# Kernel tuning notes

Hardware: AMD Instinct MI355X
Metric: run time of the kernel (lower is better)

Reference implementation:

```python
import jax, jax.numpy as jnp
import numpy as np

N, EM, EW, L, S = 20000, 100000, 25000, 128, 6


def _mlp(x, W1, b1, W2, b2, g, beta):
    # Linear -> ReLU -> Linear -> LayerNorm
    h = jax.nn.relu(x @ W1 + b1) @ W2 + b2
    mu = jnp.mean(h, axis=-1, keepdims=True)
    var = jnp.mean((h - mu) ** 2, axis=-1, keepdims=True)
    return g * (h - mu) * jax.lax.rsqrt(var + 1e-5) + beta


def _scatter_mean(attr, recv, n):
    s = jax.ops.segment_sum(attr, recv, num_segments=n)
    c = jax.ops.segment_sum(jnp.ones((attr.shape[0], 1), attr.dtype), recv, num_segments=n)
    return s / jnp.maximum(c, 1.0)


def setup_inputs() -> dict:
    key = jax.random.key(0)
    ks = jax.random.split(key, 16)

    def w(k, shape, fan_in):
        return (jax.random.normal(k, shape, jnp.float32) / np.sqrt(fan_in).astype(np.float32))

    inp = {
        'x': jax.random.normal(ks[0], (N, L), jnp.float32),
        'mesh_edge_attr': jax.random.normal(ks[1], (EM, L), jnp.float32),
        'world_edge_attr': jax.random.normal(ks[2], (EW, L), jnp.float32),
        'mesh_edge_index': jax.random.randint(ks[3], (2, EM), 0, N),
        'world_edge_index': jax.random.randint(ks[4], (2, EW), 0, N),
    }
    i = 5
    for pre in ('me', 'we', 'nd'):
        inp[pre + '_W1'] = w(ks[i], (S, 3 * L, L), 3 * L); i += 1
        inp[pre + '_b1'] = jnp.zeros((S, L), jnp.float32)
        inp[pre + '_W2'] = w(ks[i], (S, L, L), L); i += 1
        inp[pre + '_b2'] = jnp.zeros((S, L), jnp.float32)
        inp[pre + '_g'] = jnp.ones((S, L), jnp.float32)
        inp[pre + '_beta'] = jnp.zeros((S, L), jnp.float32)
    return inp


def reference(x, mesh_edge_attr, world_edge_attr, mesh_edge_index, world_edge_index,
              me_W1, me_b1, me_W2, me_b2, me_g, me_beta,
              we_W1, we_b1, we_W2, we_b2, we_g, we_beta,
              nd_W1, nd_b1, nd_W2, nd_b2, nd_g, nd_beta):
    ms, mr = mesh_edge_index[0], mesh_edge_index[1]
    ws, wr = world_edge_index[0], world_edge_index[1]
    n = x.shape[0]

    def step(carry, p):
        x, mea, wea = carry
        (mW1, mb1, mW2, mb2, mg, mbe,
         wW1, wb1, wW2, wb2, wg, wbe,
         nW1, nb1, nW2, nb2, ng, nbe) = p
        # EdgeModel: gather + concat + MLP, residual into edge attrs
        mea = mea + _mlp(jnp.concatenate([x[ms], x[mr], mea], axis=-1), mW1, mb1, mW2, mb2, mg, mbe)
        wea = wea + _mlp(jnp.concatenate([x[ws], x[wr], wea], axis=-1), wW1, wb1, wW2, wb2, wg, wbe)
        # NodeModel: scatter-mean over both edge sets + concat + MLP, residual
        agg = jnp.concatenate([x, _scatter_mean(mea, mr, n), _scatter_mean(wea, wr, n)], axis=-1)
        x = x + _mlp(agg, nW1, nb1, nW2, nb2, ng, nbe)
        return (x, mea, wea), None

    params = (me_W1, me_b1, me_W2, me_b2, me_g, me_beta,
              we_W1, we_b1, we_W2, we_b2, we_g, we_beta,
              nd_W1, nd_b1, nd_W2, nd_b2, nd_g, nd_beta)
    (x, mea, wea), _ = jax.lax.scan(step, (x, mesh_edge_attr, world_edge_attr), params)
    return x, mea, wea
```

## Files before the change

### kernel.cpp

```cpp
#include <hip/hip_runtime.h>

constexpr int LDIM  = 128;
constexpr int NNODE = 20000;
constexpr int EM_N  = 100000;
constexpr int EW_N  = 25000;
constexpr int NSTEP = 6;

typedef short bf16x8 __attribute__((ext_vector_type(8)));
typedef short bf16x4 __attribute__((ext_vector_type(4)));
typedef float f32x4  __attribute__((ext_vector_type(4)));

struct MlpParams {
  const short* xb;
  const float* attrIn;
  float*       attrOut;
  short*       xbOut;
  const int*   src;
  const int*   dst;
  const float* gsrc1;
  const float* gsrc2;
  const int*   off1;
  const int*   csr1;
  const int*   off2;
  const int*   csr2;
  const short* W1H;
  const short* W2H;
  const short* W2L;
  const float* b1;
  const float* b2;
  const float* gam;
  const float* bet;
  int nRows;
};

__device__ __forceinline__ short f2b(float f) {
  unsigned int u = __float_as_uint(f);
  u = (u + 0x7fffu + ((u >> 16) & 1u)) >> 16;
  return (short)u;
}
__device__ __forceinline__ float b2f(short s) {
  return __uint_as_float(((unsigned int)(unsigned short)s) << 16);
}
__device__ __forceinline__ bf16x4 cvt4(float4 a, float sc) {
  bf16x4 o;
  o[0] = f2b(a.x * sc); o[1] = f2b(a.y * sc);
  o[2] = f2b(a.z * sc); o[3] = f2b(a.w * sc);
  return o;
}
__device__ __forceinline__ bf16x4 cvt4v(f32x4 a, float sc) {
  bf16x4 o;
  o[0] = f2b(a[0] * sc); o[1] = f2b(a[1] * sc);
  o[2] = f2b(a[2] * sc); o[3] = f2b(a[3] * sc);
  return o;
}

__launch_bounds__(256, 2)
__global__ void edge_kernel(MlpParams pmA, MlpParams pmB, int blocksA) {
  const bool isA = (int)blockIdx.x < blocksA;
  const MlpParams P = isA ? pmA : pmB;
  const int bid  = isA ? (int)blockIdx.x : (int)blockIdx.x - blocksA;
  const int row0 = bid * 128;

  __shared__ __align__(16) short Abuf[128][40];
  __shared__ __align__(16) short Bhi[128][40];
  __shared__ __align__(16) short Blo[128][40];
  __shared__ __align__(16) short Hbuf[128][136];
  __shared__ float b1s[128], b2s[128], gs[128], bes[128];
  __shared__ int   idxa[128], idxb[128];
  __shared__ float sumL[2][128], sqL[2][128];
  __shared__ float muL[128], rsL[128];

  const int t = threadIdx.x;

  if (t < 128) {
    b1s[t] = P.b1[t];
    gs[t]  = P.gam[t];
    int r = row0 + t;
    idxa[t] = (r < P.nRows) ? P.src[r] : 0;
  } else {
    int t2 = t - 128;
    b2s[t2] = P.b2[t2];
    bes[t2] = P.bet[t2];
    int r = row0 + t2;
    idxb[t2] = (r < P.nRows) ? P.dst[r] : 0;
  }
  __syncthreads();

  const int l   = t & 63;
  const int wid = t >> 6;
  const int wr  = wid >> 1, wcc = wid & 1;
  const int lr  = l & 15,  lg  = l >> 4;

  const int  srow  = t >> 1, sh = t & 1;
  const int  sgRow = row0 + srow;
  const bool sval  = sgRow < P.nRows;
  const int  sgC   = sval ? sgRow : 0;
  const float vmask = sval ? 1.f : 0.f;

  const short* bx0   = P.xb + (size_t)idxa[srow] * LDIM + sh * 16;
  const short* bx1   = P.xb + (size_t)idxb[srow] * LDIM + sh * 16;
  const float* base2 = P.attrIn + (size_t)sgC * LDIM + sh * 16;

  const int wrow = t >> 1, wsh = t & 1;
  const short* w1base = P.W1H + (size_t)wrow * 384 + wsh * 16;

  f32x4 acc[4][4];
#pragma unroll
  for (int i = 0; i < 4; ++i)
#pragma unroll
    for (int j = 0; j < 4; ++j) acc[i][j] = f32x4{0.f, 0.f, 0.f, 0.f};

  const bf16x8 z8 = {0, 0, 0, 0, 0, 0, 0, 0};
  bf16x8 pB0, pB1;
  float4 pA0, pA1, pA2, pA3;
  bf16x8 pW0, pW1;
  {
    pB0 = *(const bf16x8*)bx0;
    pB1 = *(const bf16x8*)(bx0 + 8);
    pW0 = *(const bf16x8*)w1base;
    pW1 = *(const bf16x8*)(w1base + 8);
  }

#pragma unroll
  for (int kc = 0; kc < 12; ++kc) {
    const int seg = kc >> 2;
    if (kc > 0) __syncthreads();
    {
      if (seg < 2) {
        *(bf16x8*)&Abuf[srow][sh * 16]     = sval ? pB0 : z8;
        *(bf16x8*)&Abuf[srow][sh * 16 + 8] = sval ? pB1 : z8;
      } else {
        *(bf16x4*)&Abuf[srow][sh * 16 + 0]  = cvt4(pA0, vmask);
        *(bf16x4*)&Abuf[srow][sh * 16 + 4]  = cvt4(pA1, vmask);
        *(bf16x4*)&Abuf[srow][sh * 16 + 8]  = cvt4(pA2, vmask);
        *(bf16x4*)&Abuf[srow][sh * 16 + 12] = cvt4(pA3, vmask);
      }
      *(bf16x8*)&Bhi[wrow][wsh * 16]     = pW0;
      *(bf16x8*)&Bhi[wrow][wsh * 16 + 8] = pW1;
    }
    __syncthreads();
    if (kc < 11) {
      const int kn = kc + 1, segn = kn >> 2, partn = kn & 3;
      if (segn == 0) {
        pB0 = *(const bf16x8*)(bx0 + partn * 32);
        pB1 = *(const bf16x8*)(bx0 + partn * 32 + 8);
      } else if (segn == 1) {
        pB0 = *(const bf16x8*)(bx1 + partn * 32);
        pB1 = *(const bf16x8*)(bx1 + partn * 32 + 8);
      } else {
        const float4* bp = (const float4*)(base2 + partn * 32);
        pA0 = bp[0]; pA1 = bp[1]; pA2 = bp[2]; pA3 = bp[3];
      }
      pW0 = *(const bf16x8*)(w1base + kn * 32);
      pW1 = *(const bf16x8*)(w1base + kn * 32 + 8);
    }
    bf16x8 av[4], bh[4];
#pragma unroll
    for (int mi = 0; mi < 4; ++mi)
      av[mi] = *(const bf16x8*)&Abuf[wr * 64 + mi * 16 + lr][lg * 8];
#pragma unroll
    for (int ni = 0; ni < 4; ++ni)
      bh[ni] = *(const bf16x8*)&Bhi[wcc * 64 + ni * 16 + lr][lg * 8];
#pragma unroll
    for (int mi = 0; mi < 4; ++mi)
#pragma unroll
      for (int ni = 0; ni < 4; ++ni)
        acc[mi][ni] = __builtin_amdgcn_mfma_f32_16x16x32_bf16(av[mi], bh[ni], acc[mi][ni], 0, 0, 0);
  }

#pragma unroll
  for (int rt = 0; rt < 4; ++rt)
#pragma unroll
    for (int ct = 0; ct < 4; ++ct) {
      const int cc = wcc * 64 + ct * 16 + lr;
      const float bb = b1s[cc];
#pragma unroll
      for (int q = 0; q < 4; ++q) {
        const int rr = wr * 64 + rt * 16 + lg * 4 + q;
        Hbuf[rr][cc] = f2b(fmaxf(acc[rt][ct][q] + bb, 0.f));
      }
    }

  f32x4 acc2[4][4];
#pragma unroll
  for (int i = 0; i < 4; ++i)
#pragma unroll
    for (int j = 0; j < 4; ++j) acc2[i][j] = f32x4{0.f, 0.f, 0.f, 0.f};

  const short* w2hbase = P.W2H + (size_t)wrow * 128 + wsh * 16;
  const short* w2lbase = P.W2L + (size_t)wrow * 128 + wsh * 16;

  bf16x8 qh0 = *(const bf16x8*)w2hbase;
  bf16x8 qh1 = *(const bf16x8*)(w2hbase + 8);
  bf16x8 ql0 = *(const bf16x8*)w2lbase;
  bf16x8 ql1 = *(const bf16x8*)(w2lbase + 8);

#pragma unroll
  for (int kc = 0; kc < 4; ++kc) {
    __syncthreads();
    {
      *(bf16x8*)&Bhi[wrow][wsh * 16]     = qh0;
      *(bf16x8*)&Bhi[wrow][wsh * 16 + 8] = qh1;
      *(bf16x8*)&Blo[wrow][wsh * 16]     = ql0;
      *(bf16x8*)&Blo[wrow][wsh * 16 + 8] = ql1;
    }
    __syncthreads();
    if (kc < 3) {
      qh0 = *(const bf16x8*)(w2hbase + (kc + 1) * 32);
      qh1 = *(const bf16x8*)(w2hbase + (kc + 1) * 32 + 8);
      ql0 = *(const bf16x8*)(w2lbase + (kc + 1) * 32);
      ql1 = *(const bf16x8*)(w2lbase + (kc + 1) * 32 + 8);
    }
    bf16x8 av2[4], bh2[4], bl2[4];
#pragma unroll
    for (int rt = 0; rt < 4; ++rt)
      av2[rt] = *(const bf16x8*)&Hbuf[wr * 64 + rt * 16 + lr][kc * 32 + lg * 8];
#pragma unroll
    for (int ct = 0; ct < 4; ++ct) {
      bh2[ct] = *(const bf16x8*)&Bhi[wcc * 64 + ct * 16 + lr][lg * 8];
      bl2[ct] = *(const bf16x8*)&Blo[wcc * 64 + ct * 16 + lr][lg * 8];
    }
#pragma unroll
    for (int rt = 0; rt < 4; ++rt)
#pragma unroll
      for (int ct = 0; ct < 4; ++ct) {
        acc2[rt][ct] = __builtin_amdgcn_mfma_f32_16x16x32_bf16(av2[rt], bl2[ct], acc2[rt][ct], 0, 0, 0);
        acc2[rt][ct] = __builtin_amdgcn_mfma_f32_16x16x32_bf16(av2[rt], bh2[ct], acc2[rt][ct], 0, 0, 0);
      }
  }

  float s1[4][4], s2[4][4];
#pragma unroll
  for (int rt = 0; rt < 4; ++rt)
#pragma unroll
    for (int q = 0; q < 4; ++q) { s1[rt][q] = 0.f; s2[rt][q] = 0.f; }
#pragma unroll
  for (int rt = 0; rt < 4; ++rt)
#pragma unroll
    for (int ct = 0; ct < 4; ++ct) {
      const float bb = b2s[wcc * 64 + ct * 16 + lr];
#pragma unroll
      for (int q = 0; q < 4; ++q) {
        float v = acc2[rt][ct][q] + bb;
        acc2[rt][ct][q] = v;
        s1[rt][q] += v;
        s2[rt][q] += v * v;
      }
    }
#pragma unroll
  for (int m = 1; m < 16; m <<= 1) {
#pragma unroll
    for (int rt = 0; rt < 4; ++rt)
#pragma unroll
      for (int q = 0; q < 4; ++q) {
        s1[rt][q] += __shfl_xor(s1[rt][q], m);
        s2[rt][q] += __shfl_xor(s2[rt][q], m);
      }
  }
  __syncthreads();
  {
    const int rt = lr >> 2, q = lr & 3;
    const int rr = wr * 64 + rt * 16 + lg * 4 + q;
    sumL[wcc][rr] = s1[rt][q];
    sqL[wcc][rr]  = s2[rt][q];
  }
  __syncthreads();
  if (t < 128) {
    const float tot = sumL[0][t] + sumL[1][t];
    const float tsq = sqL[0][t] + sqL[1][t];
    const float mu  = tot * (1.0f / 128.0f);
    const float var = tsq * (1.0f / 128.0f) - mu * mu;
    muL[t] = mu;
    rsL[t] = rsqrtf(var + 1e-5f);
  }
  __syncthreads();

#pragma unroll
  for (int rt = 0; rt < 4; ++rt) {
#pragma unroll
    for (int q = 0; q < 4; ++q) {
      const int rr = wr * 64 + rt * 16 + lg * 4 + q;
      const int grow = row0 + rr;
      if (grow < P.nRows) {
        const float mu = muL[rr], rs = rsL[rr];
        const float* rin = P.attrIn + (size_t)grow * LDIM;
        float* rout = P.attrOut + (size_t)grow * LDIM;
#pragma unroll
        for (int ct = 0; ct < 4; ++ct) {
          const int cc = wcc * 64 + ct * 16 + lr;
          rout[cc] = gs[cc] * (acc2[rt][ct][q] - mu) * rs + bes[cc] + rin[cc];
        }
      }
    }
  }
}

__launch_bounds__(256, 2)
__global__ void node_kernel(MlpParams P) {
  const int bid  = (int)blockIdx.x;
  const int row0 = bid * 128;

  __shared__ __align__(16) short Abuf[128][40];
  __shared__ __align__(16) short Bhi[128][40];
  __shared__ __align__(16) short Blo[128][40];
  __shared__ __align__(16) short Hbuf[128][136];
  __shared__ float b1s[128], b2s[128], gs[128], bes[128];
  __shared__ float sumL[2][128], sqL[2][128];
  __shared__ float muL[128], rsL[128];

  const int t = threadIdx.x;
  if (t < 128) { b1s[t] = P.b1[t]; gs[t] = P.gam[t]; }
  else         { b2s[t - 128] = P.b2[t - 128]; bes[t - 128] = P.bet[t - 128]; }

  const int l   = t & 63;
  const int wid = t >> 6;
  const int wr  = wid >> 1, wcc = wid & 1;
  const int lr  = l & 15,  lg  = l >> 4;

  const int  srow  = t >> 1, sh = t & 1;
  const int  sgRow = row0 + srow;
  const bool sval  = sgRow < P.nRows;
  const int  sgC   = sval ? sgRow : 0;

  const int wrow = t >> 1, wsh = t & 1;
  const short* w1base = P.W1H + (size_t)wrow * 384 + wsh * 16;
  const short* xrow   = P.xb + (size_t)sgC * LDIM + sh * 16;
  const bf16x8 z8 = {0, 0, 0, 0, 0, 0, 0, 0};

  f32x4 acc[4][4];
#pragma unroll
  for (int i = 0; i < 4; ++i)
#pragma unroll
    for (int j = 0; j < 4; ++j) acc[i][j] = f32x4{0.f, 0.f, 0.f, 0.f};

  f32x4 g[16];
#pragma unroll
  for (int j = 0; j < 16; ++j) g[j] = f32x4{0.f, 0.f, 0.f, 0.f};
  float scm = 1.f;
  {
    int beg = 0, end = 0;
    if (sval) { beg = P.off1[sgRow]; end = P.off1[sgRow + 1]; }
    for (int i = beg; i < end; ++i) {
      const float* er = P.gsrc1 + (size_t)P.csr1[i] * LDIM + sh * 16;
#pragma unroll
      for (int part = 0; part < 4; ++part) {
        const f32x4* p = (const f32x4*)(er + part * 32);
#pragma unroll
        for (int j = 0; j < 4; ++j) g[part * 4 + j] += p[j];
      }
    }
    scm = 1.0f / (float)max(end - beg, 1);
  }

  __syncthreads();

  float scw = 1.f;
#pragma unroll
  for (int kc = 0; kc < 12; ++kc) {
    const int seg = kc >> 2, part = kc & 3;
    if (kc > 0) __syncthreads();
    {
      if (seg == 0) {
        const bf16x8* xp = (const bf16x8*)(xrow + part * 32);
        *(bf16x8*)&Abuf[srow][sh * 16]     = sval ? xp[0] : z8;
        *(bf16x8*)&Abuf[srow][sh * 16 + 8] = sval ? xp[1] : z8;
      } else {
        const float sc = (seg == 1) ? scm : scw;
        *(bf16x4*)&Abuf[srow][sh * 16 + 0]  = cvt4v(g[part * 4 + 0], sc);
        *(bf16x4*)&Abuf[srow][sh * 16 + 4]  = cvt4v(g[part * 4 + 1], sc);
        *(bf16x4*)&Abuf[srow][sh * 16 + 8]  = cvt4v(g[part * 4 + 2], sc);
        *(bf16x4*)&Abuf[srow][sh * 16 + 12] = cvt4v(g[part * 4 + 3], sc);
      }
      const short* wsrc = w1base + kc * 32;
      *(bf16x8*)&Bhi[wrow][wsh * 16]     = *(const bf16x8*)wsrc;
      *(bf16x8*)&Bhi[wrow][wsh * 16 + 8] = *(const bf16x8*)(wsrc + 8);
      if (kc == 7) {
#pragma unroll
        for (int j = 0; j < 16; ++j) g[j] = f32x4{0.f, 0.f, 0.f, 0.f};
        int beg = 0, end = 0;
        if (sval) { beg = P.off2[sgRow]; end = P.off2[sgRow + 1]; }
        for (int i = beg; i < end; ++i) {
          const float* er = P.gsrc2 + (size_t)P.csr2[i] * LDIM + sh * 16;
#pragma unroll
          for (int pp = 0; pp < 4; ++pp) {
            const f32x4* p = (const f32x4*)(er + pp * 32);
#pragma unroll
            for (int j = 0; j < 4; ++j) g[pp * 4 + j] += p[j];
          }
        }
        scw = 1.0f / (float)max(end - beg, 1);
      }
    }
    __syncthreads();
    bf16x8 av[4], bh[4];
#pragma unroll
    for (int mi = 0; mi < 4; ++mi)
      av[mi] = *(const bf16x8*)&Abuf[wr * 64 + mi * 16 + lr][lg * 8];
#pragma unroll
    for (int ni = 0; ni < 4; ++ni)
      bh[ni] = *(const bf16x8*)&Bhi[wcc * 64 + ni * 16 + lr][lg * 8];
#pragma unroll
    for (int mi = 0; mi < 4; ++mi)
#pragma unroll
      for (int ni = 0; ni < 4; ++ni)
        acc[mi][ni] = __builtin_amdgcn_mfma_f32_16x16x32_bf16(av[mi], bh[ni], acc[mi][ni], 0, 0, 0);
  }

#pragma unroll
  for (int rt = 0; rt < 4; ++rt)
#pragma unroll
    for (int ct = 0; ct < 4; ++ct) {
      const int cc = wcc * 64 + ct * 16 + lr;
      const float bb = b1s[cc];
#pragma unroll
      for (int q = 0; q < 4; ++q) {
        const int rr = wr * 64 + rt * 16 + lg * 4 + q;
        Hbuf[rr][cc] = f2b(fmaxf(acc[rt][ct][q] + bb, 0.f));
      }
    }

  f32x4 acc2[4][4];
#pragma unroll
  for (int i = 0; i < 4; ++i)
#pragma unroll
    for (int j = 0; j < 4; ++j) acc2[i][j] = f32x4{0.f, 0.f, 0.f, 0.f};

  const short* w2hbase = P.W2H + (size_t)wrow * 128 + wsh * 16;
  const short* w2lbase = P.W2L + (size_t)wrow * 128 + wsh * 16;
  bf16x8 qh0 = *(const bf16x8*)w2hbase;
  bf16x8 qh1 = *(const bf16x8*)(w2hbase + 8);
  bf16x8 ql0 = *(const bf16x8*)w2lbase;
  bf16x8 ql1 = *(const bf16x8*)(w2lbase + 8);

#pragma unroll
  for (int kc = 0; kc < 4; ++kc) {
    __syncthreads();
    {
      *(bf16x8*)&Bhi[wrow][wsh * 16]     = qh0;
      *(bf16x8*)&Bhi[wrow][wsh * 16 + 8] = qh1;
      *(bf16x8*)&Blo[wrow][wsh * 16]     = ql0;
      *(bf16x8*)&Blo[wrow][wsh * 16 + 8] = ql1;
    }
    __syncthreads();
    if (kc < 3) {
      qh0 = *(const bf16x8*)(w2hbase + (kc + 1) * 32);
      qh1 = *(const bf16x8*)(w2hbase + (kc + 1) * 32 + 8);
      ql0 = *(const bf16x8*)(w2lbase + (kc + 1) * 32);
      ql1 = *(const bf16x8*)(w2lbase + (kc + 1) * 32 + 8);
    }
    bf16x8 av2[4], bh2[4], bl2[4];
#pragma unroll
    for (int rt = 0; rt < 4; ++rt)
      av2[rt] = *(const bf16x8*)&Hbuf[wr * 64 + rt * 16 + lr][kc * 32 + lg * 8];
#pragma unroll
    for (int ct = 0; ct < 4; ++ct) {
      bh2[ct] = *(const bf16x8*)&Bhi[wcc * 64 + ct * 16 + lr][lg * 8];
      bl2[ct] = *(const bf16x8*)&Blo[wcc * 64 + ct * 16 + lr][lg * 8];
    }
#pragma unroll
    for (int rt = 0; rt < 4; ++rt)
#pragma unroll
      for (int ct = 0; ct < 4; ++ct) {
        acc2[rt][ct] = __builtin_amdgcn_mfma_f32_16x16x32_bf16(av2[rt], bl2[ct], acc2[rt][ct], 0, 0, 0);
        acc2[rt][ct] = __builtin_amdgcn_mfma_f32_16x16x32_bf16(av2[rt], bh2[ct], acc2[rt][ct], 0, 0, 0);
      }
  }

  float s1[4][4], s2[4][4];
#pragma unroll
  for (int rt = 0; rt < 4; ++rt)
#pragma unroll
    for (int q = 0; q < 4; ++q) { s1[rt][q] = 0.f; s2[rt][q] = 0.f; }
#pragma unroll
  for (int rt = 0; rt < 4; ++rt)
#pragma unroll
    for (int ct = 0; ct < 4; ++ct) {
      const float bb = b2s[wcc * 64 + ct * 16 + lr];
#pragma unroll
      for (int q = 0; q < 4; ++q) {
        float v = acc2[rt][ct][q] + bb;
        acc2[rt][ct][q] = v;
        s1[rt][q] += v;
        s2[rt][q] += v * v;
      }
    }
#pragma unroll
  for (int m = 1; m < 16; m <<= 1) {
#pragma unroll
    for (int rt = 0; rt < 4; ++rt)
#pragma unroll
      for (int q = 0; q < 4; ++q) {
        s1[rt][q] += __shfl_xor(s1[rt][q], m);
        s2[rt][q] += __shfl_xor(s2[rt][q], m);
      }
  }
  __syncthreads();
  {
    const int rt = lr >> 2, q = lr & 3;
    const int rr = wr * 64 + rt * 16 + lg * 4 + q;
    sumL[wcc][rr] = s1[rt][q];
    sqL[wcc][rr]  = s2[rt][q];
  }
  __syncthreads();
  if (t < 128) {
    const float tot = sumL[0][t] + sumL[1][t];
    const float tsq = sqL[0][t] + sqL[1][t];
    const float mu  = tot * (1.0f / 128.0f);
    const float var = tsq * (1.0f / 128.0f) - mu * mu;
    muL[t] = mu;
    rsL[t] = rsqrtf(var + 1e-5f);
  }
  __syncthreads();

#pragma unroll
  for (int rt = 0; rt < 4; ++rt) {
#pragma unroll
    for (int q = 0; q < 4; ++q) {
      const int rr = wr * 64 + rt * 16 + lg * 4 + q;
      const int grow = row0 + rr;
      if (grow < P.nRows) {
        const float mu = muL[rr], rs = rsL[rr];
        const float* rin = P.attrIn + (size_t)grow * LDIM;
        float* rout = P.attrOut + (size_t)grow * LDIM;
        short* xbo  = P.xbOut + (size_t)grow * LDIM;
#pragma unroll
        for (int ct = 0; ct < 4; ++ct) {
          const int cc = wcc * 64 + ct * 16 + lr;
          const float o = gs[cc] * (acc2[rt][ct][q] - mu) * rs + bes[cc] + rin[cc];
          rout[cc] = o;
          xbo[cc] = f2b(o);
        }
      }
    }
  }
}

__global__ void prep_weights(const float* w1a, const float* w1b, const float* w1c,
                             const float* w2a, const float* w2b, const float* w2c,
                             short* w1h, short* w2h, short* w2l) {
  int i = blockIdx.x * 256 + threadIdx.x;
  constexpr int N1 = 18 * 128 * 384;
  constexpr int N2 = 18 * 128 * 128;
  if (i < N1) {
    int g = i / (128 * 384);
    int rem = i - g * (128 * 384);
    int n = rem / 384, k = rem - n * 384;
    int m = g / 6, s = g - m * 6;
    const float* src = (m == 0) ? w1a : (m == 1) ? w1b : w1c;
    w1h[i] = f2b(src[(size_t)s * (384 * 128) + (size_t)k * 128 + n]);
  } else if (i < N1 + N2) {
    int j = i - N1;
    int g = j / (128 * 128);
    int rem = j - g * (128 * 128);
    int n = rem / 128, k = rem - n * 128;
    int m = g / 6, s = g - m * 6;
    const float* src = (m == 0) ? w2a : (m == 1) ? w2b : w2c;
    float f = src[(size_t)s * (128 * 128) + (size_t)k * 128 + n];
    short hi = f2b(f);
    w2h[j] = hi;
    w2l[j] = f2b(f - b2f(hi));
  }
}

__global__ void prep_xb(const float* x, short* xb) {
  int i = blockIdx.x * 256 + threadIdx.x;
  if (i < NNODE * LDIM) xb[i] = f2b(x[i]);
}

__global__ void prep_deg(const int* mr, const int* wrcv, int* degm, int* degw) {
  int i = blockIdx.x * 256 + threadIdx.x;
  if (i < EM_N) atomicAdd(&degm[mr[i]], 1);
  else if (i < EM_N + EW_N) atomicAdd(&degw[wrcv[i - EM_N]], 1);
}

__global__ void prep_scan(const int* degm, const int* degw, int* moff, int* woff) {
  __shared__ int part[256];
  const int t = threadIdx.x;
  constexpr int NPT = (NNODE + 255) / 256;
#pragma unroll 1
  for (int pass = 0; pass < 2; ++pass) {
    const int* deg = pass == 0 ? degm : degw;
    int* off = pass == 0 ? moff : woff;
    int s = 0;
    for (int i = 0; i < NPT; ++i) {
      int n = t * NPT + i;
      if (n < NNODE) s += deg[n];
    }
    part[t] = s;
    __syncthreads();
    for (int d = 1; d < 256; d <<= 1) {
      int v = (t >= d) ? part[t - d] : 0;
      __syncthreads();
      part[t] += v;
      __syncthreads();
    }
    int base = (t == 0) ? 0 : part[t - 1];
    for (int i = 0; i < NPT; ++i) {
      int n = t * NPT + i;
      if (n < NNODE) { off[n] = base; base += deg[n]; }
    }
    if (t == 255) off[NNODE] = base;
    __syncthreads();
  }
}

__global__ void prep_fill(const int* mr, const int* wrcv,
                          const int* moff, const int* woff,
                          int* mcur, int* wcur, int* mcsr, int* wcsr) {
  int i = blockIdx.x * 256 + threadIdx.x;
  if (i < EM_N) {
    int d = mr[i];
    int pos = moff[d] + atomicAdd(&mcur[d], 1);
    mcsr[pos] = i;
  } else if (i < EM_N + EW_N) {
    int j = i - EM_N;
    int d = wrcv[j];
    int pos = woff[d] + atomicAdd(&wcur[d], 1);
    wcsr[pos] = j;
  }
}

extern "C" void kernel_launch(void* const* d_in, const int* in_sizes, int n_in,
                              void* d_out, int out_size, void* d_ws, size_t ws_size,
                              hipStream_t stream) {
  (void)in_sizes; (void)n_in; (void)out_size; (void)ws_size;
  const float* x_in   = (const float*)d_in[0];
  const float* mea_in = (const float*)d_in[1];
  const float* wea_in = (const float*)d_in[2];
  const int*   mei    = (const int*)d_in[3];
  const int*   wei    = (const int*)d_in[4];
  const float* W1s[3] = { (const float*)d_in[5],  (const float*)d_in[11], (const float*)d_in[17] };
  const float* B1s[3] = { (const float*)d_in[6],  (const float*)d_in[12], (const float*)d_in[18] };
  const float* W2s[3] = { (const float*)d_in[7],  (const float*)d_in[13], (const float*)d_in[19] };
  const float* B2s[3] = { (const float*)d_in[8],  (const float*)d_in[14], (const float*)d_in[20] };
  const float* Gs[3]  = { (const float*)d_in[9],  (const float*)d_in[15], (const float*)d_in[21] };
  const float* Be[3]  = { (const float*)d_in[10], (const float*)d_in[16], (const float*)d_in[22] };

  float* xo  = (float*)d_out;
  float* meo = xo  + (size_t)NNODE * LDIM;
  float* weo = meo + (size_t)EM_N * LDIM;

  int*   degm = (int*)d_ws;
  int*   degw = degm + NNODE;
  int*   mcur = degw + NNODE;
  int*   wcur = mcur + NNODE;
  int*   moff = wcur + NNODE;
  int*   woff = moff + (NNODE + 1);
  int*   mcsr = woff + (NNODE + 1);
  int*   wcsr = mcsr + EM_N;
  short* w1h  = (short*)(wcsr + EW_N);
  short* w2h  = w1h + (size_t)18 * 128 * 384;
  short* w2l  = w2h + (size_t)18 * 128 * 128;
  short* xb   = w2l + (size_t)18 * 128 * 128;

  hipMemsetAsync(d_ws, 0, (size_t)4 * NNODE * 4, stream);

  {
    int tot = 18 * 128 * 384 + 18 * 128 * 128;
    prep_weights<<<dim3((tot + 255) / 256), 256, 0, stream>>>(
        W1s[0], W1s[1], W1s[2], W2s[0], W2s[1], W2s[2], w1h, w2h, w2l);
  }
  prep_xb<<<dim3((NNODE * LDIM + 255) / 256), 256, 0, stream>>>(x_in, xb);
  prep_deg<<<dim3((EM_N + EW_N + 255) / 256), 256, 0, stream>>>(mei + EM_N, wei + EW_N, degm, degw);
  prep_scan<<<dim3(1), 256, 0, stream>>>(degm, degw, moff, woff);
  prep_fill<<<dim3((EM_N + EW_N + 255) / 256), 256, 0, stream>>>(
      mei + EM_N, wei + EW_N, moff, woff, mcur, wcur, mcsr, wcsr);

  const int MB = (EM_N + 127) / 128;
  const int WB = (EW_N + 127) / 128;
  const int NB = (NNODE + 127) / 128;

  const float* mc = mea_in;
  const float* wc = wea_in;
  const float* xc = x_in;

  for (int s = 0; s < NSTEP; ++s) {
    MlpParams pm{}, pw{}, pn{};

    pm.xb = xb; pm.attrIn = mc; pm.attrOut = meo;
    pm.src = mei; pm.dst = mei + EM_N;
    pm.W1H = w1h + (size_t)(0 * 6 + s) * 128 * 384;
    pm.W2H = w2h + (size_t)(0 * 6 + s) * 128 * 128;
    pm.W2L = w2l + (size_t)(0 * 6 + s) * 128 * 128;
    pm.b1 = B1s[0] + s * LDIM; pm.b2 = B2s[0] + s * LDIM;
    pm.gam = Gs[0] + s * LDIM; pm.bet = Be[0] + s * LDIM;
    pm.nRows = EM_N;

    pw.xb = xb; pw.attrIn = wc; pw.attrOut = weo;
    pw.src = wei; pw.dst = wei + EW_N;
    pw.W1H = w1h + (size_t)(1 * 6 + s) * 128 * 384;
    pw.W2H = w2h + (size_t)(1 * 6 + s) * 128 * 128;
    pw.W2L = w2l + (size_t)(1 * 6 + s) * 128 * 128;
    pw.b1 = B1s[1] + s * LDIM; pw.b2 = B2s[1] + s * LDIM;
    pw.gam = Gs[1] + s * LDIM; pw.bet = Be[1] + s * LDIM;
    pw.nRows = EW_N;

    edge_kernel<<<dim3(MB + WB), 256, 0, stream>>>(pm, pw, MB);

    pn.xb = xb; pn.attrIn = xc; pn.attrOut = xo; pn.xbOut = xb;
    pn.gsrc1 = meo; pn.gsrc2 = weo;
    pn.off1 = moff; pn.csr1 = mcsr;
    pn.off2 = woff; pn.csr2 = wcsr;
    pn.W1H = w1h + (size_t)(2 * 6 + s) * 128 * 384;
    pn.W2H = w2h + (size_t)(2 * 6 + s) * 128 * 128;
    pn.W2L = w2l + (size_t)(2 * 6 + s) * 128 * 128;
    pn.b1 = B1s[2] + s * LDIM; pn.b2 = B2s[2] + s * LDIM;
    pn.gam = Gs[2] + s * LDIM; pn.bet = Be[2] + s * LDIM;
    pn.nRows = NNODE;

    node_kernel<<<dim3(NB), 256, 0, stream>>>(pn);

    mc = meo; wc = weo; xc = xo;
  }
}
```

Measured before the change: 891.0 us.

## Keep edge attributes sorted by receiver so node aggregation reads contiguously

Edge attributes are permuted once into receiver-sorted order in workspace, and sender/receiver index arrays are permuted to match. The edge kernel updates the sorted buffers in place and scatters to the original output order only on the last step. The node kernel then sums each node's incoming edges as contiguous rows instead of gathering through the CSR index. In exchange it needs a large workspace, one extra permute pass, and an extra scattered write on the final step; if the workspace is too small it falls back to the old path.

```diff
diff --git a/kernel.cpp b/kernel.cpp
--- a/kernel.cpp
+++ b/kernel.cpp
@@ -17,6 +17,8 @@
   short*       xbOut;
   const int*   src;
   const int*   dst;
+  const int*   oidx;
+  float*       origOut;
   const float* gsrc1;
   const float* gsrc2;
   const int*   off1;
@@ -285,16 +287,21 @@
         const float mu = muL[rr], rs = rsL[rr];
         const float* rin = P.attrIn + (size_t)grow * LDIM;
         float* rout = P.attrOut + (size_t)grow * LDIM;
+        float* rout2 = nullptr;
+        if (P.origOut) rout2 = P.origOut + (size_t)P.oidx[grow] * LDIM;
 #pragma unroll
         for (int ct = 0; ct < 4; ++ct) {
           const int cc = wcc * 64 + ct * 16 + lr;
-          rout[cc] = gs[cc] * (acc2[rt][ct][q] - mu) * rs + bes[cc] + rin[cc];
+          const float o = gs[cc] * (acc2[rt][ct][q] - mu) * rs + bes[cc] + rin[cc];
+          rout[cc] = o;
+          if (rout2) rout2[cc] = o;
         }
       }
     }
   }
 }
 
+template<bool CONTIG>
 __launch_bounds__(256, 2)
 __global__ void node_kernel(MlpParams P) {
   const int bid  = (int)blockIdx.x;
@@ -341,7 +348,8 @@
     int beg = 0, end = 0;
     if (sval) { beg = P.off1[sgRow]; end = P.off1[sgRow + 1]; }
     for (int i = beg; i < end; ++i) {
-      const float* er = P.gsrc1 + (size_t)P.csr1[i] * LDIM + sh * 16;
+      const size_t r = CONTIG ? (size_t)i : (size_t)P.csr1[i];
+      const float* er = P.gsrc1 + r * LDIM + sh * 16;
 #pragma unroll
       for (int part = 0; part < 4; ++part) {
         const f32x4* p = (const f32x4*)(er + part * 32);
@@ -380,7 +388,8 @@
         int beg = 0, end = 0;
         if (sval) { beg = P.off2[sgRow]; end = P.off2[sgRow + 1]; }
         for (int i = beg; i < end; ++i) {
-          const float* er = P.gsrc2 + (size_t)P.csr2[i] * LDIM + sh * 16;
+          const size_t r = CONTIG ? (size_t)i : (size_t)P.csr2[i];
+          const float* er = P.gsrc2 + r * LDIM + sh * 16;
 #pragma unroll
           for (int pp = 0; pp < 4; ++pp) {
             const f32x4* p = (const f32x4*)(er + pp * 32);
@@ -604,26 +613,46 @@
   }
 }
 
-__global__ void prep_fill(const int* mr, const int* wrcv,
+__global__ void prep_fill(const int* ms, const int* mr, const int* wsnd, const int* wrcv,
                           const int* moff, const int* woff,
-                          int* mcur, int* wcur, int* mcsr, int* wcsr) {
+                          int* mcur, int* wcur, int* mcsr, int* wcsr,
+                          int* psm, int* pdm, int* psw, int* pdw) {
   int i = blockIdx.x * 256 + threadIdx.x;
   if (i < EM_N) {
     int d = mr[i];
     int pos = moff[d] + atomicAdd(&mcur[d], 1);
     mcsr[pos] = i;
+    psm[pos] = ms[i];
+    pdm[pos] = d;
   } else if (i < EM_N + EW_N) {
     int j = i - EM_N;
     int d = wrcv[j];
     int pos = woff[d] + atomicAdd(&wcur[d], 1);
     wcsr[pos] = j;
+    psw[pos] = wsnd[j];
+    pdw[pos] = d;
+  }
+}
+
+__global__ void prep_permute(const float* src_m, const float* src_w,
+                             const int* mcsr, const int* wcsr,
+                             float* dst_m, float* dst_w) {
+  long i = (long)blockIdx.x * 256 + threadIdx.x;
+  const long NM4 = (long)EM_N * 32, NW4 = (long)EW_N * 32;
+  if (i < NM4) {
+    long pos = i >> 5, c = i & 31;
+    ((float4*)dst_m)[pos * 32 + c] = ((const float4*)src_m)[(size_t)mcsr[pos] * 32 + c];
+  } else if (i < NM4 + NW4) {
+    long j = i - NM4;
+    long pos = j >> 5, c = j & 31;
+    ((float4*)dst_w)[pos * 32 + c] = ((const float4*)src_w)[(size_t)wcsr[pos] * 32 + c];
   }
 }
 
 extern "C" void kernel_launch(void* const* d_in, const int* in_sizes, int n_in,
                               void* d_out, int out_size, void* d_ws, size_t ws_size,
                               hipStream_t stream) {
-  (void)in_sizes; (void)n_in; (void)out_size; (void)ws_size;
+  (void)in_sizes; (void)n_in; (void)out_size;
   const float* x_in   = (const float*)d_in[0];
   const float* mea_in = (const float*)d_in[1];
   const float* wea_in = (const float*)d_in[2];
@@ -640,20 +669,30 @@
   float* meo = xo  + (size_t)NNODE * LDIM;
   float* weo = meo + (size_t)EM_N * LDIM;
 
-  int*   degm = (int*)d_ws;
-  int*   degw = degm + NNODE;
-  int*   mcur = degw + NNODE;
-  int*   wcur = mcur + NNODE;
-  int*   moff = wcur + NNODE;
-  int*   woff = moff + (NNODE + 1);
-  int*   mcsr = woff + (NNODE + 1);
-  int*   wcsr = mcsr + EM_N;
-  short* w1h  = (short*)(wcsr + EW_N);
-  short* w2h  = w1h + (size_t)18 * 128 * 384;
-  short* w2l  = w2h + (size_t)18 * 128 * 128;
-  short* xb   = w2l + (size_t)18 * 128 * 128;
-
-  hipMemsetAsync(d_ws, 0, (size_t)4 * NNODE * 4, stream);
+  const size_t SORT_BYTES = ((size_t)EM_N + EW_N) * LDIM * 4;
+  const size_t SMALL_BYTES = (size_t)20 * 1024 * 1024;
+  const bool SORTED = ws_size >= SORT_BYTES + SMALL_BYTES;
+
+  float* msort = (float*)d_ws;
+  float* wsort = msort + (size_t)EM_N * LDIM;
+  short* w1h = SORTED ? (short*)(wsort + (size_t)EW_N * LDIM) : (short*)d_ws;
+  short* w2h = w1h + (size_t)18 * 128 * 384;
+  short* w2l = w2h + (size_t)18 * 128 * 128;
+  short* xb  = w2l + (size_t)18 * 128 * 128;
+  int* degm = (int*)(xb + (size_t)NNODE * LDIM);
+  int* degw = degm + NNODE;
+  int* mcur = degw + NNODE;
+  int* wcur = mcur + NNODE;
+  int* moff = wcur + NNODE;
+  int* woff = moff + (NNODE + 1);
+  int* mcsr = woff + (NNODE + 1);
+  int* wcsr = mcsr + EM_N;
+  int* psm  = wcsr + EW_N;
+  int* pdm  = psm + EM_N;
+  int* psw  = pdm + EM_N;
+  int* pdw  = psw + EW_N;
+
+  hipMemsetAsync(degm, 0, (size_t)4 * NNODE * 4, stream);
 
   {
     int tot = 18 * 128 * 384 + 18 * 128 * 128;
@@ -664,7 +703,13 @@
   prep_deg<<<dim3((EM_N + EW_N + 255) / 256), 256, 0, stream>>>(mei + EM_N, wei + EW_N, degm, degw);
   prep_scan<<<dim3(1), 256, 0, stream>>>(degm, degw, moff, woff);
   prep_fill<<<dim3((EM_N + EW_N + 255) / 256), 256, 0, stream>>>(
-      mei + EM_N, wei + EW_N, moff, woff, mcur, wcur, mcsr, wcsr);
+      mei, mei + EM_N, wei, wei + EW_N, moff, woff, mcur, wcur, mcsr, wcsr,
+      psm, pdm, psw, pdw);
+  if (SORTED) {
+    long tot4 = ((long)EM_N + EW_N) * 32;
+    prep_permute<<<dim3((unsigned)((tot4 + 255) / 256)), 256, 0, stream>>>(
+        mea_in, wea_in, mcsr, wcsr, msort, wsort);
+  }
 
   const int MB = (EM_N + 127) / 128;
   const int WB = (EW_N + 127) / 128;
@@ -676,9 +721,9 @@
 
   for (int s = 0; s < NSTEP; ++s) {
     MlpParams pm{}, pw{}, pn{};
-
-    pm.xb = xb; pm.attrIn = mc; pm.attrOut = meo;
-    pm.src = mei; pm.dst = mei + EM_N;
+    const bool last = (s == NSTEP - 1);
+
+    pm.xb = xb;
     pm.W1H = w1h + (size_t)(0 * 6 + s) * 128 * 384;
     pm.W2H = w2h + (size_t)(0 * 6 + s) * 128 * 128;
     pm.W2L = w2l + (size_t)(0 * 6 + s) * 128 * 128;
@@ -686,8 +731,7 @@
     pm.gam = Gs[0] + s * LDIM; pm.bet = Be[0] + s * LDIM;
     pm.nRows = EM_N;
 
-    pw.xb = xb; pw.attrIn = wc; pw.attrOut = weo;
-    pw.src = wei; pw.dst = wei + EW_N;
+    pw.xb = xb;
     pw.W1H = w1h + (size_t)(1 * 6 + s) * 128 * 384;
     pw.W2H = w2h + (size_t)(1 * 6 + s) * 128 * 128;
     pw.W2L = w2l + (size_t)(1 * 6 + s) * 128 * 128;
@@ -695,12 +739,24 @@
     pw.gam = Gs[1] + s * LDIM; pw.bet = Be[1] + s * LDIM;
     pw.nRows = EW_N;
 
+    if (SORTED) {
+      pm.attrIn = msort; pm.attrOut = msort;
+      pm.src = psm; pm.dst = pdm;
+      pm.oidx = mcsr; pm.origOut = last ? meo : nullptr;
+      pw.attrIn = wsort; pw.attrOut = wsort;
+      pw.src = psw; pw.dst = pdw;
+      pw.oidx = wcsr; pw.origOut = last ? weo : nullptr;
+    } else {
+      pm.attrIn = mc; pm.attrOut = meo;
+      pm.src = mei; pm.dst = mei + EM_N;
+      pw.attrIn = wc; pw.attrOut = weo;
+      pw.src = wei; pw.dst = wei + EW_N;
+    }
+
     edge_kernel<<<dim3(MB + WB), 256, 0, stream>>>(pm, pw, MB);
 
     pn.xb = xb; pn.attrIn = xc; pn.attrOut = xo; pn.xbOut = xb;
-    pn.gsrc1 = meo; pn.gsrc2 = weo;
-    pn.off1 = moff; pn.csr1 = mcsr;
-    pn.off2 = woff; pn.csr2 = wcsr;
+    pn.off1 = moff; pn.off2 = woff;
     pn.W1H = w1h + (size_t)(2 * 6 + s) * 128 * 384;
     pn.W2H = w2h + (size_t)(2 * 6 + s) * 128 * 128;
     pn.W2L = w2l + (size_t)(2 * 6 + s) * 128 * 128;
@@ -708,7 +764,14 @@
     pn.gam = Gs[2] + s * LDIM; pn.bet = Be[2] + s * LDIM;
     pn.nRows = NNODE;
 
-    node_kernel<<<dim3(NB), 256, 0, stream>>>(pn);
+    if (SORTED) {
+      pn.gsrc1 = msort; pn.gsrc2 = wsort;
+      node_kernel<true><<<dim3(NB), 256, 0, stream>>>(pn);
+    } else {
+      pn.gsrc1 = meo; pn.gsrc2 = weo;
+      pn.csr1 = mcsr; pn.csr2 = wcsr;
+      node_kernel<false><<<dim3(NB), 256, 0, stream>>>(pn);
+    }
 
     mc = meo; wc = weo; xc = xo;
   }
```

Measured after the change: 852.5 us. 1.05x faster.
